# Optimization experiments

Measured on AMD Instinct MI355X. Metric: run time of the kernel, lower is better.

## Reference

```python
import jax, jax.numpy as jnp
import numpy as np

N, V = 256, 5
D_DX, D_RX = 48, 48
C = 128            # code_dim
DEMO_F, DEMO_D = 32, 64
DT, NH, DFF = 256, 8, 2048
REP, HID = 128, 256
NE, NC = 2, 64
VOC_DX = (1000, 5000, 20000)
VOC_RX = (100, 500, 2000, 5000)
NEG = -1e20

def _ln(x, s, b):
    m = jnp.mean(x, -1, keepdims=True)
    v = jnp.var(x, -1, keepdims=True)
    return (x - m) / jnp.sqrt(v + 1e-5) * s + b

def _pe(seq, d):
    pos = jnp.arange(seq, dtype=jnp.float32)[:, None]
    i = jnp.arange(0, d, 2, dtype=jnp.float32)
    ang = pos / jnp.power(10000.0, i / d)
    pe = jnp.zeros((seq, d), jnp.float32)
    pe = pe.at[:, 0::2].set(jnp.sin(ang))
    pe = pe.at[:, 1::2].set(jnp.cos(ang))
    return pe

def _mha(x, qw, qb, ow_, ob_):
    n, s, d = x.shape
    hd = d // NH
    q, k, v = jnp.split(x @ qw + qb, 3, axis=-1)
    q = q.reshape(n, s, NH, hd); k = k.reshape(n, s, NH, hd); v = v.reshape(n, s, NH, hd)
    att = jax.nn.softmax(jnp.einsum('bqhd,bkhd->bhqk', q, k) / jnp.sqrt(jnp.float32(hd)), axis=-1)
    return jnp.einsum('bhqk,bkhd->bqhd', att, v).reshape(n, s, d) @ ow_ + ob_

def _enc_layer(x, qw, qb, ow_, ob_, l1s, l1b, f1w, f1b, f2w, f2b, l2s, l2b):
    x = _ln(x + _mha(x, qw, qb, ow_, ob_), l1s, l1b)            # post-norm, as nn.TransformerEncoderLayer default
    ff = jnp.maximum(x @ f1w + f1b, 0.0) @ f2w + f2b
    return _ln(x + ff, l2s, l2b)

def setup_inputs() -> dict:
    key = jax.random.key(0)
    ks = iter(jax.random.split(key, 96))
    def nrm(shape, scale=0.02):
        return jax.random.normal(next(ks), shape, jnp.float32) * scale
    def zeros(shape): return jnp.zeros(shape, jnp.float32)
    def ones(shape): return jnp.ones(shape, jnp.float32)
    inp = {}
    inp['x_dx_l1'] = jax.random.randint(next(ks), (N, V, D_DX), 0, VOC_DX[0])
    inp['x_dx_l2'] = jax.random.randint(next(ks), (N, V, D_DX), 0, VOC_DX[1])
    inp['x_dx_l3'] = jax.random.randint(next(ks), (N, V, D_DX), 0, VOC_DX[2])
    inp['x_rx_l1'] = jax.random.randint(next(ks), (N, V, D_RX), 0, VOC_RX[0])
    inp['x_rx_l2'] = jax.random.randint(next(ks), (N, V, D_RX), 0, VOC_RX[1])
    inp['x_rx_l3'] = jax.random.randint(next(ks), (N, V, D_RX), 0, VOC_RX[2])
    inp['x_rx_l4'] = jax.random.randint(next(ks), (N, V, D_RX), 0, VOC_RX[3])
    inp['x_demo'] = jax.random.normal(next(ks), (N, V, DEMO_F), jnp.float32)
    inp['W_demo'] = nrm((DEMO_F, DEMO_D)); inp['b_demo'] = zeros((DEMO_D,))
    inp['E_dx1'] = nrm((VOC_DX[0], C)); inp['E_dx2'] = nrm((VOC_DX[1], C)); inp['E_dx3'] = nrm((VOC_DX[2], C))
    inp['E_rx1'] = nrm((VOC_RX[0], C)); inp['E_rx2'] = nrm((VOC_RX[1], C))
    inp['E_rx3'] = nrm((VOC_RX[2], C)); inp['E_rx4'] = nrm((VOC_RX[3], C))
    inp['We_dx'] = nrm((2 * C, 1)); inp['be_dx'] = zeros((1,))
    inp['We_rx'] = nrm((2 * C, 1)); inp['be_rx'] = zeros((1,))
    inp['Wev_dx'] = nrm((C, 1)); inp['bev_dx'] = zeros((1,))
    inp['Wev_rx'] = nrm((C, 1)); inp['bev_rx'] = zeros((1,))
    inp['Wcv'] = nrm((REP, 1)); inp['bcv'] = zeros((1,))
    inp['enc_w1'] = nrm((DEMO_D + C, DT)); inp['enc_b1'] = zeros((DT,))
    inp['qkv_w'] = nrm((4, DT, 3 * DT)); inp['qkv_b'] = zeros((4, 3 * DT))
    inp['ow'] = nrm((4, DT, DT)); inp['ob'] = zeros((4, DT))
    inp['ln1s'] = ones((4, DT)); inp['ln1b'] = zeros((4, DT))
    inp['ff1w'] = nrm((4, DT, DFF)); inp['ff1b'] = zeros((4, DFF))
    inp['ff2w'] = nrm((4, DFF, DT)); inp['ff2b'] = zeros((4, DT))
    inp['ln2s'] = ones((4, DT)); inp['ln2b'] = zeros((4, DT))
    inp['enc_w2'] = nrm((DT, REP)); inp['enc_b2'] = zeros((REP,))
    inp['mlp_w'] = nrm((REP, REP // 2)); inp['mlp_b'] = zeros((REP // 2,))
    inp['mlp2_w'] = nrm((REP // 2, REP // 2)); inp['mlp2_b'] = zeros((REP // 2,))
    inp['fc1w'] = nrm((NE, REP, HID)); inp['fc1b'] = zeros((NE, HID))
    inp['fc2w'] = nrm((NE, HID, HID // 2)); inp['fc2b'] = zeros((NE, HID // 2))
    inp['fc3w'] = nrm((NE, HID // 2, NC)); inp['fc3b'] = zeros((NE, NC))
    return inp

def reference(x_dx_l1, x_dx_l2, x_dx_l3, x_rx_l1, x_rx_l2, x_rx_l3, x_rx_l4, x_demo,
              W_demo, b_demo, E_dx1, E_dx2, E_dx3, E_rx1, E_rx2, E_rx3, E_rx4,
              We_dx, be_dx, We_rx, be_rx, Wev_dx, bev_dx, Wev_rx, bev_rx, Wcv, bcv,
              enc_w1, enc_b1, qkv_w, qkv_b, ow, ob, ln1s, ln1b, ff1w, ff1b, ff2w, ff2b,
              ln2s, ln2b, enc_w2, enc_b2, mlp_w, mlp_b, mlp2_w, mlp2_b,
              fc1w, fc1b, fc2w, fc2b, fc3w, fc3b):
    # ---- GRAM context vectors (dropout is identity at inference) ----
    emb_dx = jnp.stack([E_dx1[x_dx_l1], E_dx2[x_dx_l2], E_dx3[x_dx_l3]], axis=-2)          # [N,V,D,3,C]
    cat_dx = jnp.concatenate([jnp.broadcast_to(emb_dx[..., 2:3, :], emb_dx.shape), emb_dx], axis=-1)
    en_dx = jnp.maximum(cat_dx @ We_dx + be_dx, 0.0)                                       # [N,V,D,3,1]
    en_dx = jnp.where((x_dx_l1 != 0)[..., None, None], en_dx, NEG)
    att_dx = jax.nn.softmax(en_dx, axis=-2)
    cv_dx = jnp.einsum('nvdr,nvdrc->nvdc', att_dx[..., 0], emb_dx)                          # [N,V,D,C]

    emb_rx = jnp.stack([E_rx1[x_rx_l1], E_rx2[x_rx_l2], E_rx3[x_rx_l3], E_rx4[x_rx_l4]], axis=-2)  # [N,V,D,4,C]
    cat_rx = jnp.concatenate([jnp.broadcast_to(emb_rx[..., 3:4, :], emb_rx.shape), emb_rx], axis=-1)
    en_rx = jnp.maximum(cat_rx @ We_rx + be_rx, 0.0)
    en_rx = jnp.where((x_rx_l1 != 0)[..., None, None], en_rx, NEG)
    att_rx = jax.nn.softmax(en_rx, axis=-2)
    cv_rx = jnp.einsum('nvdr,nvdrc->nvdc', att_rx[..., 0], emb_rx)

    # ---- visit-level attention pooling over concatenated codes ----
    context = jnp.concatenate([cv_dx, cv_rx], axis=-2)                                      # [N,V,Ddx+Drx,C]
    ev_dx = jnp.where((x_dx_l1 != 0)[..., None], cv_dx @ Wev_dx + bev_dx, NEG)
    ev_rx = jnp.where((x_rx_l1 != 0)[..., None], cv_rx @ Wev_rx + bev_rx, NEG)
    att_v = jax.nn.softmax(jnp.concatenate([ev_dx, ev_rx], axis=-2), axis=-2)               # [N,V,M,1]
    ccv = jnp.einsum('nvm,nvmc->nvc', att_v[..., 0], context)                               # [N,V,C]

    # ---- shared transformer encoder ----
    demo = jnp.maximum(x_demo @ W_demo + b_demo, 0.0)
    x = jnp.concatenate([demo, ccv], axis=-1) @ enc_w1 + enc_b1
    x = x + _pe(V, DT)[None]
    for i in range(4):
        x = _enc_layer(x, qkv_w[i], qkv_b[i], ow[i], ob[i], ln1s[i], ln1b[i],
                       ff1w[i], ff1b[i], ff2w[i], ff2b[i], ln2s[i], ln2b[i])
    enc = x @ enc_w2 + enc_b2                                                               # [N,V,REP]

    # ---- visit compression ----
    a = jax.nn.softmax(enc @ Wcv + bcv, axis=-2)                                            # [N,V,1]
    civ = jnp.einsum('nv,nvc->nc', a[..., 0], enc)                                          # [N,REP]

    ph = jnp.maximum(civ @ mlp_w + mlp_b, 0.0) @ mlp2_w + mlp2_b                            # [N,REP/2]

    # ---- per-event FC heads (vectorized over events) ----
    h = jnp.maximum(jnp.einsum('nc,ech->neh', civ, fc1w) + fc1b, 0.0)
    h = jnp.maximum(jnp.einsum('neh,ehk->nek', h, fc2w) + fc2b, 0.0)
    out = jax.nn.sigmoid(jnp.einsum('nek,ekm->nem', h, fc3w) + fc3b)                        # [N,NE,NC]
    return out, civ, ph
```

## Files before the change

### kernel.cpp

```cpp
#include <hip/hip_runtime.h>
#include <hip/hip_bf16.h>
#include <math.h>

#define N_PAT 256
#define VIS   5
#define NV    (N_PAT*VIS)
#define DD    48
#define CD    128
#define DT    256
#define NHD   8
#define HD    32
#define DFF   2048
#define REP   128

#define GF_BIAS 1
#define GF_RELU 2
#define GF_PE   4

typedef __attribute__((ext_vector_type(8))) short short8v;
typedef __attribute__((ext_vector_type(4))) float f32x4;

__device__ __forceinline__ unsigned short f2b(float f) {
    unsigned u = __float_as_uint(f);
    return (unsigned short)((u + 0x7fffu + ((u >> 16) & 1u)) >> 16);
}

__global__ void pe_kernel(float* __restrict__ pe) {
    int pos = blockIdx.x, c = threadIdx.x;
    int j = c >> 1;
    float ang = (float)pos / powf(10000.f, (2.f * (float)j) / 256.f);
    pe[pos * DT + c] = (c & 1) ? cosf(ang) : sinf(ang);
}

__global__ __launch_bounds__(256) void wconv_kernel(
    const float* __restrict__ in, unsigned short* __restrict__ out, int K, int N)
{
    __shared__ float t[32][33];
    const float* src = in + (size_t)blockIdx.z * K * N;
    unsigned short* dst = out + (size_t)blockIdx.z * N * K;
    int k0 = blockIdx.y * 32, n0 = blockIdx.x * 32;
    int tx = threadIdx.x & 31, ty = threadIdx.x >> 5;
    #pragma unroll
    for (int r = ty; r < 32; r += 8) t[r][tx] = src[(size_t)(k0 + r) * N + n0 + tx];
    __syncthreads();
    #pragma unroll
    for (int r = ty; r < 32; r += 8) dst[(size_t)(n0 + r) * K + k0 + tx] = f2b(t[tx][r]);
}

__global__ __launch_bounds__(256) void proj_kernel(
    const float* __restrict__ E, const float* __restrict__ W_lo,
    const float* __restrict__ W_hi, const float* __restrict__ Wev,
    int nrows, float* __restrict__ out)
{
    const int row = blockIdx.x * 4 + (threadIdx.x >> 6);
    const int lane = threadIdx.x & 63;
    if (row >= nrows) return;
    float2 e   = *(const float2*)(E + (size_t)row * CD + lane * 2);
    float2 whi = *(const float2*)(W_hi + lane * 2);
    float2 wlo = *(const float2*)(W_lo + lane * 2);
    float2 wev = *(const float2*)(Wev + lane * 2);
    float ph = e.x * whi.x + e.y * whi.y;
    float pl = e.x * wlo.x + e.y * wlo.y;
    float pw = e.x * wev.x + e.y * wev.y;
    #pragma unroll
    for (int off = 32; off; off >>= 1) {
        ph += __shfl_xor(ph, off, 64);
        pl += __shfl_xor(pl, off, 64);
        pw += __shfl_xor(pw, off, 64);
    }
    if (lane == 0) {
        out[(size_t)row * 4 + 0] = ph;
        out[(size_t)row * 4 + 1] = pl;
        out[(size_t)row * 4 + 2] = pw;
        out[(size_t)row * 4 + 3] = 0.f;
    }
}

__global__ __launch_bounds__(256) void gram_kernel(
    const int* __restrict__ xd1, const int* __restrict__ xd2, const int* __restrict__ xd3,
    const int* __restrict__ xr1, const int* __restrict__ xr2, const int* __restrict__ xr3,
    const int* __restrict__ xr4,
    const float* __restrict__ Ed1, const float* __restrict__ Ed2, const float* __restrict__ Ed3,
    const float* __restrict__ Er1, const float* __restrict__ Er2, const float* __restrict__ Er3,
    const float* __restrict__ Er4,
    const float* __restrict__ pd1, const float* __restrict__ pd2, const float* __restrict__ pd3,
    const float* __restrict__ pr1, const float* __restrict__ pr2, const float* __restrict__ pr3,
    const float* __restrict__ pr4,
    const float* __restrict__ be_dx, const float* __restrict__ be_rx,
    const float* __restrict__ bev_dx, const float* __restrict__ bev_rx,
    float* __restrict__ ccv)
{
    __shared__ float aw[96][4];
    __shared__ float ev[96];
    __shared__ int   sidx[96][4];
    __shared__ float part[4][128];
    const int nv   = blockIdx.x;
    const int tid  = threadIdx.x;
    const int wave = tid >> 6, lane = tid & 63;
    const int base = nv * DD;

    if (tid < 48) {
        const int d = tid;
        const int i1 = xd1[base + d], i2 = xd2[base + d], i3 = xd3[base + d];
        sidx[d][0] = i1; sidx[d][1] = i2; sidx[d][2] = i3;
        float4 q1 = *(const float4*)(pd1 + (size_t)i1 * 4);
        float4 q2 = *(const float4*)(pd2 + (size_t)i2 * 4);
        float4 q3 = *(const float4*)(pd3 + (size_t)i3 * 4);
        const float be = be_dx[0];
        const float p0 = q3.y;
        float s1 = fmaxf(p0 + q1.x + be, 0.f);
        float s2 = fmaxf(p0 + q2.x + be, 0.f);
        float s3 = fmaxf(p0 + q3.x + be, 0.f);
        float a1, a2, a3;
        if (i1 != 0) {
            float mx = fmaxf(s1, fmaxf(s2, s3));
            a1 = expf(s1 - mx); a2 = expf(s2 - mx); a3 = expf(s3 - mx);
        } else {
            a1 = a2 = a3 = 1.f;
        }
        float inv = 1.f / (a1 + a2 + a3);
        a1 *= inv; a2 *= inv; a3 *= inv;
        aw[d][0] = a1; aw[d][1] = a2; aw[d][2] = a3; aw[d][3] = 0.f;
        ev[d] = (i1 != 0) ? (a1 * q1.z + a2 * q2.z + a3 * q3.z + bev_dx[0]) : -1e20f;
    } else if (tid >= 64 && tid < 112) {
        const int d = tid - 64;
        const int i1 = xr1[base + d], i2 = xr2[base + d], i3 = xr3[base + d], i4 = xr4[base + d];
        const int m = 48 + d;
        sidx[m][0] = i1; sidx[m][1] = i2; sidx[m][2] = i3; sidx[m][3] = i4;
        float4 q1 = *(const float4*)(pr1 + (size_t)i1 * 4);
        float4 q2 = *(const float4*)(pr2 + (size_t)i2 * 4);
        float4 q3 = *(const float4*)(pr3 + (size_t)i3 * 4);
        float4 q4 = *(const float4*)(pr4 + (size_t)i4 * 4);
        const float be = be_rx[0];
        const float p0 = q4.y;
        float s1 = fmaxf(p0 + q1.x + be, 0.f);
        float s2 = fmaxf(p0 + q2.x + be, 0.f);
        float s3 = fmaxf(p0 + q3.x + be, 0.f);
        float s4 = fmaxf(p0 + q4.x + be, 0.f);
        float a1, a2, a3, a4;
        if (i1 != 0) {
            float mx = fmaxf(fmaxf(s1, s2), fmaxf(s3, s4));
            a1 = expf(s1 - mx); a2 = expf(s2 - mx); a3 = expf(s3 - mx); a4 = expf(s4 - mx);
        } else {
            a1 = a2 = a3 = a4 = 1.f;
        }
        float inv = 1.f / (a1 + a2 + a3 + a4);
        aw[m][0] = a1 * inv; aw[m][1] = a2 * inv; aw[m][2] = a3 * inv; aw[m][3] = a4 * inv;
        ev[m] = (i1 != 0) ? ((a1 * q1.z + a2 * q2.z + a3 * q3.z + a4 * q4.z) * inv + bev_rx[0])
                          : -1e20f;
    }
    __syncthreads();

    if (wave == 0) {
        float a = ev[lane];
        float b = (lane < 32) ? ev[64 + lane] : -3.0e38f;
        float mx = fmaxf(a, b);
        #pragma unroll
        for (int off = 32; off; off >>= 1) mx = fmaxf(mx, __shfl_xor(mx, off, 64));
        float ea = expf(a - mx);
        float eb = (lane < 32) ? expf(b - mx) : 0.f;
        float s = ea + eb;
        #pragma unroll
        for (int off = 32; off; off >>= 1) s += __shfl_xor(s, off, 64);
        float inv = 1.f / s;
        ev[lane] = ea * inv;
        if (lane < 32) ev[64 + lane] = eb * inv;
    }
    __syncthreads();

    if (tid < 96) {
        float av = ev[tid];
        aw[tid][0] *= av; aw[tid][1] *= av; aw[tid][2] *= av; aw[tid][3] *= av;
    }
    __syncthreads();

    float accx = 0.f, accy = 0.f;
    const int co = lane * 2;
    for (int m = wave; m < 96; m += 4) {
        if (m < 48) {
            int i1 = sidx[m][0], i2 = sidx[m][1], i3 = sidx[m][2];
            float2 e1 = *(const float2*)(Ed1 + (size_t)i1 * CD + co);
            float2 e2 = *(const float2*)(Ed2 + (size_t)i2 * CD + co);
            float2 e3 = *(const float2*)(Ed3 + (size_t)i3 * CD + co);
            float w1 = aw[m][0], w2 = aw[m][1], w3 = aw[m][2];
            accx += w1 * e1.x + w2 * e2.x + w3 * e3.x;
            accy += w1 * e1.y + w2 * e2.y + w3 * e3.y;
        } else {
            int i1 = sidx[m][0], i2 = sidx[m][1], i3 = sidx[m][2], i4 = sidx[m][3];
            float2 e1 = *(const float2*)(Er1 + (size_t)i1 * CD + co);
            float2 e2 = *(const float2*)(Er2 + (size_t)i2 * CD + co);
            float2 e3 = *(const float2*)(Er3 + (size_t)i3 * CD + co);
            float2 e4 = *(const float2*)(Er4 + (size_t)i4 * CD + co);
            float w1 = aw[m][0], w2 = aw[m][1], w3 = aw[m][2], w4 = aw[m][3];
            accx += w1 * e1.x + w2 * e2.x + w3 * e3.x + w4 * e4.x;
            accy += w1 * e1.y + w2 * e2.y + w3 * e3.y + w4 * e4.y;
        }
    }
    part[wave][co]     = accx;
    part[wave][co + 1] = accy;
    __syncthreads();
    if (tid < CD) {
        ccv[(size_t)nv * CD + tid] =
            part[0][tid] + part[1][tid] + part[2][tid] + part[3][tid];
    }
}

__global__ __launch_bounds__(192) void build_x0(
    const float* __restrict__ x_demo, const float* __restrict__ W_demo,
    const float* __restrict__ b_demo, const float* __restrict__ ccv,
    unsigned short* __restrict__ A0bf)
{
    int row = blockIdx.x, j = threadIdx.x;
    float v;
    if (j < 64) {
        float acc = b_demo[j];
        #pragma unroll
        for (int f = 0; f < 32; ++f) acc += x_demo[row * 32 + f] * W_demo[f * 64 + j];
        v = fmaxf(acc, 0.f);
    } else {
        v = ccv[row * CD + (j - 64)];
    }
    A0bf[row * 192 + j] = f2b(v);
}

__global__ __launch_bounds__(256) void gemm_bf(
    const unsigned short* __restrict__ A, const unsigned short* __restrict__ B,
    const float* __restrict__ bias, const float* __restrict__ pe,
    float* __restrict__ Cf, unsigned short* __restrict__ Cb,
    int M, int N, int K, int flags, int kchunk)
{
    __shared__ unsigned short As[64][40];
    __shared__ unsigned short Bs[64][40];
    const int bm = blockIdx.y * 64, bn = blockIdx.x * 64;
    const int tid = threadIdx.x;
    const int wave = tid >> 6, lane = tid & 63;
    const int wr = (wave >> 1) * 32, wc = (wave & 1) * 32;
    const int l15 = lane & 15, l4 = lane >> 4;
    const int srow = tid >> 2, sk8 = (tid & 3) * 8;
    const int kbeg = blockIdx.z * kchunk, kend = kbeg + kchunk;
    f32x4 acc[2][2] = {};

    for (int k0 = kbeg; k0 < kend; k0 += 32) {
        *(short8v*)&As[srow][sk8] = *(const short8v*)(A + (size_t)(bm + srow) * K + k0 + sk8);
        *(short8v*)&Bs[srow][sk8] = *(const short8v*)(B + (size_t)(bn + srow) * K + k0 + sk8);
        __syncthreads();
        short8v a0 = *(const short8v*)&As[wr + l15][l4 * 8];
        short8v a1 = *(const short8v*)&As[wr + 16 + l15][l4 * 8];
        short8v b0 = *(const short8v*)&Bs[wc + l15][l4 * 8];
        short8v b1 = *(const short8v*)&Bs[wc + 16 + l15][l4 * 8];
        acc[0][0] = __builtin_amdgcn_mfma_f32_16x16x32_bf16(a0, b0, acc[0][0], 0, 0, 0);
        acc[0][1] = __builtin_amdgcn_mfma_f32_16x16x32_bf16(a0, b1, acc[0][1], 0, 0, 0);
        acc[1][0] = __builtin_amdgcn_mfma_f32_16x16x32_bf16(a1, b0, acc[1][0], 0, 0, 0);
        acc[1][1] = __builtin_amdgcn_mfma_f32_16x16x32_bf16(a1, b1, acc[1][1], 0, 0, 0);
        __syncthreads();
    }

    if (gridDim.z == 1) {
        #pragma unroll
        for (int mi = 0; mi < 2; ++mi)
            #pragma unroll
            for (int ni = 0; ni < 2; ++ni) {
                int col = bn + wc + ni * 16 + l15;
                float bz = (flags & GF_BIAS) ? bias[col] : 0.f;
                #pragma unroll
                for (int r = 0; r < 4; ++r) {
                    int row = bm + wr + mi * 16 + l4 * 4 + r;
                    float v = acc[mi][ni][r] + bz;
                    if (flags & GF_PE)   v += pe[(row % VIS) * N + col];
                    if (flags & GF_RELU) v = fmaxf(v, 0.f);
                    if (Cf) Cf[(size_t)row * N + col] = v;
                    if (Cb) Cb[(size_t)row * N + col] = f2b(v);
                }
            }
    } else {
        float* Cp = Cf + (size_t)blockIdx.z * M * N;
        #pragma unroll
        for (int mi = 0; mi < 2; ++mi)
            #pragma unroll
            for (int ni = 0; ni < 2; ++ni) {
                int col = bn + wc + ni * 16 + l15;
                #pragma unroll
                for (int r = 0; r < 4; ++r) {
                    int row = bm + wr + mi * 16 + l4 * 4 + r;
                    Cp[(size_t)row * N + col] = acc[mi][ni][r];
                }
            }
    }
}

__global__ __launch_bounds__(256) void gemm_k(
    const float* __restrict__ A, const float* __restrict__ B,
    const float* __restrict__ bias, const float* __restrict__ pe,
    float* __restrict__ C, int M, int N, int K, int flags, int kchunk)
{
    __shared__ float As[16][68];
    __shared__ float Bs[16][64];
    const int bm = blockIdx.y * 64, bn = blockIdx.x * 64;
    const int tid = threadIdx.x;
    const int tx = tid & 15, ty = tid >> 4;
    const int kbeg = blockIdx.z * kchunk;
    const int kend = kbeg + kchunk;
    const int ar  = tid >> 2, akc = (tid & 3) * 4;
    const int bbr = tid >> 4, bbc = (tid & 15) * 4;
    float acc[4][4] = {{0.f}};

    for (int k0 = kbeg; k0 < kend; k0 += 16) {
        float4 va = *(const float4*)(A + (size_t)(bm + ar) * K + k0 + akc);
        float4 vb = *(const float4*)(B + (size_t)(k0 + bbr) * N + bn + bbc);
        As[akc + 0][ar] = va.x;
        As[akc + 1][ar] = va.y;
        As[akc + 2][ar] = va.z;
        As[akc + 3][ar] = va.w;
        *(float4*)&Bs[bbr][bbc] = vb;
        __syncthreads();
        #pragma unroll
        for (int kk = 0; kk < 16; ++kk) {
            float4 a = *(const float4*)&As[kk][ty * 4];
            float4 b = *(const float4*)&Bs[kk][tx * 4];
            acc[0][0] += a.x * b.x; acc[0][1] += a.x * b.y; acc[0][2] += a.x * b.z; acc[0][3] += a.x * b.w;
            acc[1][0] += a.y * b.x; acc[1][1] += a.y * b.y; acc[1][2] += a.y * b.z; acc[1][3] += a.y * b.w;
            acc[2][0] += a.z * b.x; acc[2][1] += a.z * b.y; acc[2][2] += a.z * b.z; acc[2][3] += a.z * b.w;
            acc[3][0] += a.w * b.x; acc[3][1] += a.w * b.y; acc[3][2] += a.w * b.z; acc[3][3] += a.w * b.w;
        }
        __syncthreads();
    }

    if (gridDim.z == 1) {
        #pragma unroll
        for (int i = 0; i < 4; ++i) {
            int row = bm + ty * 4 + i;
            int col0 = bn + tx * 4;
            float4 v = *(float4*)&acc[i][0];
            if (flags & GF_BIAS) {
                const float4 bz = *(const float4*)(bias + col0);
                v.x += bz.x; v.y += bz.y; v.z += bz.z; v.w += bz.w;
            }
            if (flags & GF_PE) {
                const float4 pz = *(const float4*)(pe + (row % VIS) * N + col0);
                v.x += pz.x; v.y += pz.y; v.z += pz.z; v.w += pz.w;
            }
            if (flags & GF_RELU) {
                v.x = fmaxf(v.x, 0.f); v.y = fmaxf(v.y, 0.f);
                v.z = fmaxf(v.z, 0.f); v.w = fmaxf(v.w, 0.f);
            }
            *(float4*)(C + (size_t)row * N + col0) = v;
        }
    } else {
        float* Cp = C + (size_t)blockIdx.z * M * N;
        #pragma unroll
        for (int i = 0; i < 4; ++i) {
            int row = bm + ty * 4 + i;
            *(float4*)(Cp + (size_t)row * N + bn + tx * 4) = *(float4*)&acc[i][0];
        }
    }
}

__global__ void reduce_kernel(
    const float* __restrict__ part, int S, int MN,
    const float* __restrict__ bias,
    const float* __restrict__ resid,
    const float* __restrict__ lns, const float* __restrict__ lnb,
    int N, float* __restrict__ out, unsigned short* __restrict__ out_bf)
{
    const int row = blockIdx.x, t = threadIdx.x;
    const size_t idx = (size_t)row * N + t;
    float v = bias[t];
    for (int s = 0; s < S; ++s) v += part[(size_t)s * MN + idx];
    if (resid) v += resid[idx];
    if (lns) {
        float s1 = v, s2 = v * v;
        #pragma unroll
        for (int off = 32; off; off >>= 1) {
            s1 += __shfl_xor(s1, off, 64);
            s2 += __shfl_xor(s2, off, 64);
        }
        __shared__ float red[2][4];
        const int wave = t >> 6, lane = t & 63, nw = blockDim.x >> 6;
        if (lane == 0) { red[0][wave] = s1; red[1][wave] = s2; }
        __syncthreads();
        s1 = 0.f; s2 = 0.f;
        for (int w = 0; w < nw; ++w) { s1 += red[0][w]; s2 += red[1][w]; }
        float invn = 1.f / (float)N;
        float m    = s1 * invn;
        float var  = s2 * invn - m * m;
        float inv  = 1.f / sqrtf(var + 1e-5f);
        v = (v - m) * inv * lns[t] + lnb[t];
    }
    out[idx] = v;
    if (out_bf) out_bf[idx] = f2b(v);
}

__global__ __launch_bounds__(256) void attn_kernel(
    const float* __restrict__ qkv, unsigned short* __restrict__ out)
{
    const int n = blockIdx.x;
    const int tid = threadIdx.x;
    const int h = tid >> 5, t = tid & 31;
    const int ch = h * HD + t;
    float q[VIS], k[VIS], v[VIS];
    #pragma unroll
    for (int j = 0; j < VIS; ++j) {
        const float* row = qkv + (size_t)(n * VIS + j) * 768 + ch;
        q[j] = row[0]; k[j] = row[256]; v[j] = row[512];
    }
    const float scale = 0.1767766952966369f;
    float sm[VIS][VIS];
    #pragma unroll
    for (int qi = 0; qi < VIS; ++qi)
        #pragma unroll
        for (int ki = 0; ki < VIS; ++ki) {
            float p = q[qi] * k[ki];
            #pragma unroll
            for (int off = 16; off; off >>= 1) p += __shfl_xor(p, off, 32);
            sm[qi][ki] = p * scale;
        }
    #pragma unroll
    for (int qi = 0; qi < VIS; ++qi) {
        float mx = sm[qi][0];
        #pragma unroll
        for (int ki = 1; ki < VIS; ++ki) mx = fmaxf(mx, sm[qi][ki]);
        float e[VIS], sum = 0.f;
        #pragma unroll
        for (int ki = 0; ki < VIS; ++ki) { e[ki] = expf(sm[qi][ki] - mx); sum += e[ki]; }
        float inv = 1.f / sum;
        float acc = 0.f;
        #pragma unroll
        for (int ki = 0; ki < VIS; ++ki) acc += e[ki] * inv * v[ki];
        out[(size_t)(n * VIS + qi) * DT + ch] = f2b(acc);
    }
}

__global__ __launch_bounds__(128) void vc_ph_kernel(
    const float* __restrict__ enc, const float* __restrict__ Wcv, const float* __restrict__ bcv,
    const float* __restrict__ mlp_w, const float* __restrict__ mlp_b,
    const float* __restrict__ mlp2_w, const float* __restrict__ mlp2_b,
    float* __restrict__ civ_out, float* __restrict__ ph_out)
{
    const int n = blockIdx.x, t = threadIdx.x;
    const int wave = t >> 6, lane = t & 63;
    float e[VIS];
    #pragma unroll
    for (int v = 0; v < VIS; ++v) e[v] = enc[(size_t)(n * VIS + v) * REP + t];
    float w = Wcv[t];
    __shared__ float part[VIS][2];
    #pragma unroll
    for (int v = 0; v < VIS; ++v) {
        float pv = e[v] * w;
        #pragma unroll
        for (int off = 32; off; off >>= 1) pv += __shfl_xor(pv, off, 64);
        if (lane == 0) part[v][wave] = pv;
    }
    __syncthreads();
    float b0 = bcv[0];
    float sc[VIS], mx = -3e38f;
    #pragma unroll
    for (int v = 0; v < VIS; ++v) { sc[v] = part[v][0] + part[v][1] + b0; mx = fmaxf(mx, sc[v]); }
    float sum = 0.f;
    #pragma unroll
    for (int v = 0; v < VIS; ++v) { sc[v] = expf(sc[v] - mx); sum += sc[v]; }
    float inv = 1.f / sum;
    float civ = 0.f;
    #pragma unroll
    for (int v = 0; v < VIS; ++v) civ += sc[v] * inv * e[v];
    civ_out[(size_t)n * REP + t] = civ;

    __shared__ float civ_s[REP];
    __shared__ float h1_s[64];
    civ_s[t] = civ;
    __syncthreads();
    if (t < 64) {
        float acc = mlp_b[t];
        #pragma unroll 8
        for (int c = 0; c < REP; ++c) acc += civ_s[c] * mlp_w[c * 64 + t];
        h1_s[t] = fmaxf(acc, 0.f);
    }
    __syncthreads();
    if (t < 64) {
        float acc = mlp2_b[t];
        #pragma unroll 8
        for (int j = 0; j < 64; ++j) acc += h1_s[j] * mlp2_w[j * 64 + t];
        ph_out[(size_t)n * 64 + t] = acc;
    }
}

__global__ __launch_bounds__(256) void heads_kernel(
    const float* __restrict__ civ,
    const float* __restrict__ fc1w, const float* __restrict__ fc1b,
    const float* __restrict__ fc2w, const float* __restrict__ fc2b,
    const float* __restrict__ fc3w, const float* __restrict__ fc3b,
    float* __restrict__ out)
{
    const int n = blockIdx.x >> 1, e = blockIdx.x & 1;
    const int t = threadIdx.x;
    __shared__ float civ_s[REP], h1[256], h2[128];
    if (t < REP) civ_s[t] = civ[(size_t)n * REP + t];
    __syncthreads();
    {
        float acc = fc1b[e * 256 + t];
        const float* w = fc1w + (size_t)e * REP * 256;
        #pragma unroll 8
        for (int c = 0; c < REP; ++c) acc += civ_s[c] * w[c * 256 + t];
        h1[t] = fmaxf(acc, 0.f);
    }
    __syncthreads();
    if (t < 128) {
        float acc = fc2b[e * 128 + t];
        const float* w = fc2w + (size_t)e * 256 * 128;
        #pragma unroll 8
        for (int c = 0; c < 256; ++c) acc += h1[c] * w[c * 128 + t];
        h2[t] = fmaxf(acc, 0.f);
    }
    __syncthreads();
    if (t < 64) {
        float acc = fc3b[e * 64 + t];
        const float* w = fc3w + (size_t)e * 128 * 64;
        #pragma unroll 8
        for (int c = 0; c < 128; ++c) acc += h2[c] * w[c * 64 + t];
        out[(size_t)(n * 2 + e) * 64 + t] = 1.f / (1.f + expf(-acc));
    }
}

extern "C" void kernel_launch(void* const* d_in, const int* in_sizes, int n_in,
                              void* d_out, int out_size, void* d_ws, size_t ws_size,
                              hipStream_t stream) {
    const int*   xd1    = (const int*)  d_in[0];
    const int*   xd2    = (const int*)  d_in[1];
    const int*   xd3    = (const int*)  d_in[2];
    const int*   xr1    = (const int*)  d_in[3];
    const int*   xr2    = (const int*)  d_in[4];
    const int*   xr3    = (const int*)  d_in[5];
    const int*   xr4    = (const int*)  d_in[6];
    const float* x_demo = (const float*)d_in[7];
    const float* W_demo = (const float*)d_in[8];
    const float* b_demo = (const float*)d_in[9];
    const float* Ed1    = (const float*)d_in[10];
    const float* Ed2    = (const float*)d_in[11];
    const float* Ed3    = (const float*)d_in[12];
    const float* Er1    = (const float*)d_in[13];
    const float* Er2    = (const float*)d_in[14];
    const float* Er3    = (const float*)d_in[15];
    const float* Er4    = (const float*)d_in[16];
    const float* We_dx  = (const float*)d_in[17];
    const float* be_dx  = (const float*)d_in[18];
    const float* We_rx  = (const float*)d_in[19];
    const float* be_rx  = (const float*)d_in[20];
    const float* Wev_dx = (const float*)d_in[21];
    const float* bev_dx = (const float*)d_in[22];
    const float* Wev_rx = (const float*)d_in[23];
    const float* bev_rx = (const float*)d_in[24];
    const float* Wcv    = (const float*)d_in[25];
    const float* bcv    = (const float*)d_in[26];
    const float* enc_w1 = (const float*)d_in[27];
    const float* enc_b1 = (const float*)d_in[28];
    const float* qkv_w  = (const float*)d_in[29];
    const float* qkv_b  = (const float*)d_in[30];
    const float* ow     = (const float*)d_in[31];
    const float* ob     = (const float*)d_in[32];
    const float* ln1s   = (const float*)d_in[33];
    const float* ln1b   = (const float*)d_in[34];
    const float* ff1w   = (const float*)d_in[35];
    const float* ff1b   = (const float*)d_in[36];
    const float* ff2w   = (const float*)d_in[37];
    const float* ff2b   = (const float*)d_in[38];
    const float* ln2s   = (const float*)d_in[39];
    const float* ln2b   = (const float*)d_in[40];
    const float* enc_w2 = (const float*)d_in[41];
    const float* enc_b2 = (const float*)d_in[42];
    const float* mlp_w  = (const float*)d_in[43];
    const float* mlp_b  = (const float*)d_in[44];
    const float* mlp2_w = (const float*)d_in[45];
    const float* mlp2_b = (const float*)d_in[46];
    const float* fc1w   = (const float*)d_in[47];
    const float* fc1b   = (const float*)d_in[48];
    const float* fc2w   = (const float*)d_in[49];
    const float* fc2b   = (const float*)d_in[50];
    const float* fc3w   = (const float*)d_in[51];
    const float* fc3b   = (const float*)d_in[52];

    float* ws     = (float*)d_ws;
    float* pe     = ws;
    float* ccv    = pe + 1280;
    float* xbuf   = ccv + 163840;
    float* qkvbuf = xbuf + 327680;
    float* projbf = qkvbuf + 983040;
    float* enc    = projbf + 327680;
    float* buf2   = enc + 163840;
    float* ptab   = buf2 + 1310720;
    unsigned short* usb = (unsigned short*)(ptab + 134400);
    unsigned short* A0bf    = usb;
    unsigned short* xbuf_bf = A0bf + 245760;
    unsigned short* attn_bf = xbuf_bf + 327680;
    unsigned short* ff1_bf  = attn_bf + 327680;
    unsigned short* qkv_wt  = ff1_bf + 2621440;
    unsigned short* ow_t    = qkv_wt + 786432;
    unsigned short* ff1_wt  = ow_t + 262144;
    unsigned short* ff2_wt  = ff1_wt + 2097152;
    unsigned short* ew1_t   = ff2_wt + 2097152;

    float* pd1 = ptab;
    float* pd2 = pd1 + 4000;
    float* pd3 = pd2 + 20000;
    float* pr1 = pd3 + 80000;
    float* pr2 = pr1 + 400;
    float* pr3 = pr2 + 2000;
    float* pr4 = pr3 + 8000;

    pe_kernel<<<VIS, DT, 0, stream>>>(pe);

    wconv_kernel<<<dim3(24, 8, 4), 256, 0, stream>>>(qkv_w, qkv_wt, 256, 768);
    wconv_kernel<<<dim3(8, 8, 4), 256, 0, stream>>>(ow, ow_t, 256, 256);
    wconv_kernel<<<dim3(64, 8, 4), 256, 0, stream>>>(ff1w, ff1_wt, 256, 2048);
    wconv_kernel<<<dim3(8, 64, 4), 256, 0, stream>>>(ff2w, ff2_wt, 2048, 256);
    wconv_kernel<<<dim3(8, 6, 1), 256, 0, stream>>>(enc_w1, ew1_t, 192, 256);

    proj_kernel<<<(1000 + 3) / 4, 256, 0, stream>>>(Ed1, We_dx, We_dx + CD, Wev_dx, 1000, pd1);
    proj_kernel<<<(5000 + 3) / 4, 256, 0, stream>>>(Ed2, We_dx, We_dx + CD, Wev_dx, 5000, pd2);
    proj_kernel<<<(20000 + 3) / 4, 256, 0, stream>>>(Ed3, We_dx, We_dx + CD, Wev_dx, 20000, pd3);
    proj_kernel<<<(100 + 3) / 4, 256, 0, stream>>>(Er1, We_rx, We_rx + CD, Wev_rx, 100, pr1);
    proj_kernel<<<(500 + 3) / 4, 256, 0, stream>>>(Er2, We_rx, We_rx + CD, Wev_rx, 500, pr2);
    proj_kernel<<<(2000 + 3) / 4, 256, 0, stream>>>(Er3, We_rx, We_rx + CD, Wev_rx, 2000, pr3);
    proj_kernel<<<(5000 + 3) / 4, 256, 0, stream>>>(Er4, We_rx, We_rx + CD, Wev_rx, 5000, pr4);

    gram_kernel<<<NV, 256, 0, stream>>>(xd1, xd2, xd3, xr1, xr2, xr3, xr4,
                                        Ed1, Ed2, Ed3, Er1, Er2, Er3, Er4,
                                        pd1, pd2, pd3, pr1, pr2, pr3, pr4,
                                        be_dx, be_rx, bev_dx, bev_rx, ccv);
    build_x0<<<NV, 192, 0, stream>>>(x_demo, W_demo, b_demo, ccv, A0bf);

    gemm_bf<<<dim3(4, 20, 1), 256, 0, stream>>>(A0bf, ew1_t, enc_b1, pe,
                                                xbuf, xbuf_bf, NV, DT, 192,
                                                GF_BIAS | GF_PE, 192);

    for (int i = 0; i < 4; ++i) {
        gemm_bf<<<dim3(12, 20, 1), 256, 0, stream>>>(
            xbuf_bf, qkv_wt + (size_t)i * 768 * 256, qkv_b + i * 768, nullptr,
            qkvbuf, nullptr, NV, 768, DT, GF_BIAS, DT);
        attn_kernel<<<N_PAT, 256, 0, stream>>>(qkvbuf, attn_bf);
        gemm_bf<<<dim3(4, 20, 1), 256, 0, stream>>>(
            attn_bf, ow_t + (size_t)i * 256 * 256, nullptr, nullptr,
            projbf, nullptr, NV, DT, DT, 0, DT);
        reduce_kernel<<<NV, DT, 0, stream>>>(projbf, 1, NV * DT, ob + i * DT,
                                             xbuf, ln1s + i * DT, ln1b + i * DT,
                                             DT, xbuf, xbuf_bf);
        gemm_bf<<<dim3(32, 20, 1), 256, 0, stream>>>(
            xbuf_bf, ff1_wt + (size_t)i * DFF * 256, ff1b + i * DFF, nullptr,
            nullptr, ff1_bf, NV, DFF, DT, GF_BIAS | GF_RELU, DT);
        gemm_bf<<<dim3(4, 20, 4), 256, 0, stream>>>(
            ff1_bf, ff2_wt + (size_t)i * 256 * DFF, nullptr, nullptr,
            buf2, nullptr, NV, DT, DFF, 0, 512);
        reduce_kernel<<<NV, DT, 0, stream>>>(buf2, 4, NV * DT, ff2b + i * DT,
                                             xbuf, ln2s + i * DT, ln2b + i * DT,
                                             DT, xbuf, xbuf_bf);
    }

    gemm_k<<<dim3(2, 20, 8), 256, 0, stream>>>(xbuf, enc_w2, nullptr, nullptr, buf2,
                                               NV, REP, DT, 0, 32);
    reduce_kernel<<<NV, REP, 0, stream>>>(buf2, 8, NV * REP, enc_b2,
                                          nullptr, nullptr, nullptr, REP, enc, nullptr);

    float* civ_out = (float*)d_out + 32768;
    float* ph_out  = (float*)d_out + 65536;
    vc_ph_kernel<<<N_PAT, 128, 0, stream>>>(enc, Wcv, bcv, mlp_w, mlp_b, mlp2_w, mlp2_b,
                                            civ_out, ph_out);
    heads_kernel<<<N_PAT * 2, 256, 0, stream>>>(civ_out, fc1w, fc1b, fc2w, fc2b, fc3w, fc3b,
                                                (float*)d_out);
}
```

Measured before the change: 477.8 us.

## Fuse prep kernels, attention with out-proj and LayerNorm, and final reduce

Merges the PE and seven projection launches into one prep kernel, and the weight conversions into one batched launch that drops the out-proj conversion. Build_x0 is folded into gram_kernel. The attention kernel now also does the out-projection in fp32 from shared memory plus bias, residual and LayerNorm, replacing an MFMA GEMM and a reduce launch per layer. The final split-K reduce moves into vc_ph_kernel. This cuts launch count and intermediate buffers, but the out-projection now runs as scalar FP32 FMAs on one block per patient (256 blocks) instead of matrix cores.

```diff
diff --git a/kernel.cpp b/kernel.cpp
--- a/kernel.cpp
+++ b/kernel.cpp
@@ -8,7 +8,6 @@
 #define DD    48
 #define CD    128
 #define DT    256
-#define NHD   8
 #define HD    32
 #define DFF   2048
 #define REP   128
@@ -25,39 +24,41 @@
     return (unsigned short)((u + 0x7fffu + ((u >> 16) & 1u)) >> 16);
 }
 
-__global__ void pe_kernel(float* __restrict__ pe) {
-    int pos = blockIdx.x, c = threadIdx.x;
-    int j = c >> 1;
-    float ang = (float)pos / powf(10000.f, (2.f * (float)j) / 256.f);
-    pe[pos * DT + c] = (c & 1) ? cosf(ang) : sinf(ang);
-}
-
-__global__ __launch_bounds__(256) void wconv_kernel(
-    const float* __restrict__ in, unsigned short* __restrict__ out, int K, int N)
-{
-    __shared__ float t[32][33];
-    const float* src = in + (size_t)blockIdx.z * K * N;
-    unsigned short* dst = out + (size_t)blockIdx.z * N * K;
-    int k0 = blockIdx.y * 32, n0 = blockIdx.x * 32;
-    int tx = threadIdx.x & 31, ty = threadIdx.x >> 5;
-    #pragma unroll
-    for (int r = ty; r < 32; r += 8) t[r][tx] = src[(size_t)(k0 + r) * N + n0 + tx];
-    __syncthreads();
-    #pragma unroll
-    for (int r = ty; r < 32; r += 8) dst[(size_t)(n0 + r) * K + k0 + tx] = f2b(t[tx][r]);
-}
-
-__global__ __launch_bounds__(256) void proj_kernel(
-    const float* __restrict__ E, const float* __restrict__ W_lo,
-    const float* __restrict__ W_hi, const float* __restrict__ Wev,
-    int nrows, float* __restrict__ out)
-{
-    const int row = blockIdx.x * 4 + (threadIdx.x >> 6);
+__global__ __launch_bounds__(256) void prep_kernel(
+    const float* __restrict__ Ed1, const float* __restrict__ Ed2, const float* __restrict__ Ed3,
+    const float* __restrict__ Er1, const float* __restrict__ Er2, const float* __restrict__ Er3,
+    const float* __restrict__ Er4,
+    const float* __restrict__ We_dx, const float* __restrict__ We_rx,
+    const float* __restrict__ Wev_dx, const float* __restrict__ Wev_rx,
+    float* __restrict__ pe,
+    float* __restrict__ pd1, float* __restrict__ pd2, float* __restrict__ pd3,
+    float* __restrict__ pr1, float* __restrict__ pr2, float* __restrict__ pr3,
+    float* __restrict__ pr4)
+{
+    const int b = blockIdx.x;
+    if (b < VIS) {
+        int c = threadIdx.x, j = c >> 1;
+        float ang = (float)b / powf(10000.f, (2.f * (float)j) / 256.f);
+        pe[b * DT + c] = (c & 1) ? cosf(ang) : sinf(ang);
+        return;
+    }
+    const int g = (b - VIS) * 4 + (threadIdx.x >> 6);
     const int lane = threadIdx.x & 63;
-    if (row >= nrows) return;
-    float2 e   = *(const float2*)(E + (size_t)row * CD + lane * 2);
-    float2 whi = *(const float2*)(W_hi + lane * 2);
-    float2 wlo = *(const float2*)(W_lo + lane * 2);
+    if (g >= 33600) return;
+    const float* E; float* out; int loc; int isdx;
+    if      (g < 1000)  { E = Ed1; out = pd1; loc = g;          isdx = 1; }
+    else if (g < 6000)  { E = Ed2; out = pd2; loc = g - 1000;   isdx = 1; }
+    else if (g < 26000) { E = Ed3; out = pd3; loc = g - 6000;   isdx = 1; }
+    else if (g < 26100) { E = Er1; out = pr1; loc = g - 26000;  isdx = 0; }
+    else if (g < 26600) { E = Er2; out = pr2; loc = g - 26100;  isdx = 0; }
+    else if (g < 28600) { E = Er3; out = pr3; loc = g - 26600;  isdx = 0; }
+    else                { E = Er4; out = pr4; loc = g - 28600;  isdx = 0; }
+    const float* Wlo = isdx ? We_dx : We_rx;
+    const float* Whi = Wlo + CD;
+    const float* Wev = isdx ? Wev_dx : Wev_rx;
+    float2 e   = *(const float2*)(E + (size_t)loc * CD + lane * 2);
+    float2 whi = *(const float2*)(Whi + lane * 2);
+    float2 wlo = *(const float2*)(Wlo + lane * 2);
     float2 wev = *(const float2*)(Wev + lane * 2);
     float ph = e.x * whi.x + e.y * whi.y;
     float pl = e.x * wlo.x + e.y * wlo.y;
@@ -69,11 +70,46 @@
         pw += __shfl_xor(pw, off, 64);
     }
     if (lane == 0) {
-        out[(size_t)row * 4 + 0] = ph;
-        out[(size_t)row * 4 + 1] = pl;
-        out[(size_t)row * 4 + 2] = pw;
-        out[(size_t)row * 4 + 3] = 0.f;
-    }
+        out[(size_t)loc * 4 + 0] = ph;
+        out[(size_t)loc * 4 + 1] = pl;
+        out[(size_t)loc * 4 + 2] = pw;
+        out[(size_t)loc * 4 + 3] = 0.f;
+    }
+}
+
+__global__ __launch_bounds__(256) void wconv_all(
+    const float* __restrict__ qkv_w, unsigned short* __restrict__ qkv_wt,
+    const float* __restrict__ ff1w,  unsigned short* __restrict__ ff1_wt,
+    const float* __restrict__ ff2w,  unsigned short* __restrict__ ff2_wt,
+    const float* __restrict__ ew1,   unsigned short* __restrict__ ew1_t)
+{
+    __shared__ float t[32][33];
+    int b = blockIdx.x;
+    const float* src; unsigned short* dst; int K, N, ky, nx;
+    if (b < 768) {
+        int mat = b / 192, r = b % 192; ky = r / 24; nx = r % 24;
+        K = 256; N = 768;
+        src = qkv_w + (size_t)mat * K * N; dst = qkv_wt + (size_t)mat * N * K;
+    } else if (b < 2816) {
+        b -= 768; int mat = b / 512, r = b % 512; ky = r / 64; nx = r % 64;
+        K = 256; N = 2048;
+        src = ff1w + (size_t)mat * K * N; dst = ff1_wt + (size_t)mat * N * K;
+    } else if (b < 4864) {
+        b -= 2816; int mat = b / 512, r = b % 512; ky = r / 8; nx = r % 8;
+        K = 2048; N = 256;
+        src = ff2w + (size_t)mat * K * N; dst = ff2_wt + (size_t)mat * N * K;
+    } else {
+        b -= 4864; ky = b / 8; nx = b % 8;
+        K = 192; N = 256;
+        src = ew1; dst = ew1_t;
+    }
+    int k0 = ky * 32, n0 = nx * 32;
+    int tx = threadIdx.x & 31, ty = threadIdx.x >> 5;
+    #pragma unroll
+    for (int r = ty; r < 32; r += 8) t[r][tx] = src[(size_t)(k0 + r) * N + n0 + tx];
+    __syncthreads();
+    #pragma unroll
+    for (int r = ty; r < 32; r += 8) dst[(size_t)(n0 + r) * K + k0 + tx] = f2b(t[tx][r]);
 }
 
 __global__ __launch_bounds__(256) void gram_kernel(
@@ -88,7 +124,9 @@
     const float* __restrict__ pr4,
     const float* __restrict__ be_dx, const float* __restrict__ be_rx,
     const float* __restrict__ bev_dx, const float* __restrict__ bev_rx,
-    float* __restrict__ ccv)
+    const float* __restrict__ x_demo, const float* __restrict__ W_demo,
+    const float* __restrict__ b_demo,
+    unsigned short* __restrict__ A0bf)
 {
     __shared__ float aw[96][4];
     __shared__ float ev[96];
@@ -200,27 +238,15 @@
     part[wave][co + 1] = accy;
     __syncthreads();
     if (tid < CD) {
-        ccv[(size_t)nv * CD + tid] =
-            part[0][tid] + part[1][tid] + part[2][tid] + part[3][tid];
-    }
-}
-
-__global__ __launch_bounds__(192) void build_x0(
-    const float* __restrict__ x_demo, const float* __restrict__ W_demo,
-    const float* __restrict__ b_demo, const float* __restrict__ ccv,
-    unsigned short* __restrict__ A0bf)
-{
-    int row = blockIdx.x, j = threadIdx.x;
-    float v;
-    if (j < 64) {
+        A0bf[(size_t)nv * 192 + 64 + tid] =
+            f2b(part[0][tid] + part[1][tid] + part[2][tid] + part[3][tid]);
+    } else if (tid >= 192) {
+        int j = tid - 192;
         float acc = b_demo[j];
         #pragma unroll
-        for (int f = 0; f < 32; ++f) acc += x_demo[row * 32 + f] * W_demo[f * 64 + j];
-        v = fmaxf(acc, 0.f);
-    } else {
-        v = ccv[row * CD + (j - 64)];
-    }
-    A0bf[row * 192 + j] = f2b(v);
+        for (int f = 0; f < 32; ++f) acc += x_demo[nv * 32 + f] * W_demo[f * 64 + j];
+        A0bf[(size_t)nv * 192 + j] = f2b(fmaxf(acc, 0.f));
+    }
 }
 
 __global__ __launch_bounds__(256) void gemm_bf(
@@ -290,8 +316,7 @@
 
 __global__ __launch_bounds__(256) void gemm_k(
     const float* __restrict__ A, const float* __restrict__ B,
-    const float* __restrict__ bias, const float* __restrict__ pe,
-    float* __restrict__ C, int M, int N, int K, int flags, int kchunk)
+    float* __restrict__ C, int M, int N, int K, int kchunk)
 {
     __shared__ float As[16][68];
     __shared__ float Bs[16][64];
@@ -325,33 +350,11 @@
         __syncthreads();
     }
 
-    if (gridDim.z == 1) {
-        #pragma unroll
-        for (int i = 0; i < 4; ++i) {
-            int row = bm + ty * 4 + i;
-            int col0 = bn + tx * 4;
-            float4 v = *(float4*)&acc[i][0];
-            if (flags & GF_BIAS) {
-                const float4 bz = *(const float4*)(bias + col0);
-                v.x += bz.x; v.y += bz.y; v.z += bz.z; v.w += bz.w;
-            }
-            if (flags & GF_PE) {
-                const float4 pz = *(const float4*)(pe + (row % VIS) * N + col0);
-                v.x += pz.x; v.y += pz.y; v.z += pz.z; v.w += pz.w;
-            }
-            if (flags & GF_RELU) {
-                v.x = fmaxf(v.x, 0.f); v.y = fmaxf(v.y, 0.f);
-                v.z = fmaxf(v.z, 0.f); v.w = fmaxf(v.w, 0.f);
-            }
-            *(float4*)(C + (size_t)row * N + col0) = v;
-        }
-    } else {
-        float* Cp = C + (size_t)blockIdx.z * M * N;
-        #pragma unroll
-        for (int i = 0; i < 4; ++i) {
-            int row = bm + ty * 4 + i;
-            *(float4*)(Cp + (size_t)row * N + bn + tx * 4) = *(float4*)&acc[i][0];
-        }
+    float* Cp = C + (size_t)blockIdx.z * M * N;
+    #pragma unroll
+    for (int i = 0; i < 4; ++i) {
+        int row = bm + ty * 4 + i;
+        *(float4*)(Cp + (size_t)row * N + bn + tx * 4) = *(float4*)&acc[i][0];
     }
 }
 
@@ -390,48 +393,98 @@
     if (out_bf) out_bf[idx] = f2b(v);
 }
 
-__global__ __launch_bounds__(256) void attn_kernel(
-    const float* __restrict__ qkv, unsigned short* __restrict__ out)
-{
+__global__ __launch_bounds__(256) void attn_proj_ln(
+    const float* __restrict__ qkv,
+    const float* __restrict__ ow,
+    const float* __restrict__ ob,
+    const float* __restrict__ lns, const float* __restrict__ lnb,
+    float* __restrict__ xbuf, unsigned short* __restrict__ xbuf_bf)
+{
+    __shared__ float attn_s[VIS][DT];
+    __shared__ float red[VIS][2][4];
     const int n = blockIdx.x;
     const int tid = threadIdx.x;
     const int h = tid >> 5, t = tid & 31;
     const int ch = h * HD + t;
-    float q[VIS], k[VIS], v[VIS];
+
+    {
+        float q[VIS], k[VIS], v[VIS];
+        #pragma unroll
+        for (int j = 0; j < VIS; ++j) {
+            const float* row = qkv + (size_t)(n * VIS + j) * 768 + ch;
+            q[j] = row[0]; k[j] = row[256]; v[j] = row[512];
+        }
+        const float scale = 0.1767766952966369f;
+        float sm[VIS][VIS];
+        #pragma unroll
+        for (int qi = 0; qi < VIS; ++qi)
+            #pragma unroll
+            for (int ki = 0; ki < VIS; ++ki) {
+                float p = q[qi] * k[ki];
+                #pragma unroll
+                for (int off = 16; off; off >>= 1) p += __shfl_xor(p, off, 32);
+                sm[qi][ki] = p * scale;
+            }
+        #pragma unroll
+        for (int qi = 0; qi < VIS; ++qi) {
+            float mx = sm[qi][0];
+            #pragma unroll
+            for (int ki = 1; ki < VIS; ++ki) mx = fmaxf(mx, sm[qi][ki]);
+            float e[VIS], sum = 0.f;
+            #pragma unroll
+            for (int ki = 0; ki < VIS; ++ki) { e[ki] = expf(sm[qi][ki] - mx); sum += e[ki]; }
+            float inv = 1.f / sum;
+            float acc = 0.f;
+            #pragma unroll
+            for (int ki = 0; ki < VIS; ++ki) acc += e[ki] * inv * v[ki];
+            attn_s[qi][ch] = acc;
+        }
+    }
+    __syncthreads();
+
+    const int c = tid;
+    float acc[VIS] = {0.f, 0.f, 0.f, 0.f, 0.f};
+    #pragma unroll 4
+    for (int k = 0; k < DT; ++k) {
+        float w = ow[(size_t)k * DT + c];
+        #pragma unroll
+        for (int j = 0; j < VIS; ++j) acc[j] += attn_s[j][k] * w;
+    }
+    float bz = ob[c];
+    float v[VIS];
+    #pragma unroll
+    for (int j = 0; j < VIS; ++j)
+        v[j] = acc[j] + bz + xbuf[(size_t)(n * VIS + j) * DT + c];
+
+    const int wave = tid >> 6, lane = tid & 63;
     #pragma unroll
     for (int j = 0; j < VIS; ++j) {
-        const float* row = qkv + (size_t)(n * VIS + j) * 768 + ch;
-        q[j] = row[0]; k[j] = row[256]; v[j] = row[512];
-    }
-    const float scale = 0.1767766952966369f;
-    float sm[VIS][VIS];
-    #pragma unroll
-    for (int qi = 0; qi < VIS; ++qi)
-        #pragma unroll
-        for (int ki = 0; ki < VIS; ++ki) {
-            float p = q[qi] * k[ki];
-            #pragma unroll
-            for (int off = 16; off; off >>= 1) p += __shfl_xor(p, off, 32);
-            sm[qi][ki] = p * scale;
+        float s1 = v[j], s2 = v[j] * v[j];
+        #pragma unroll
+        for (int off = 32; off; off >>= 1) {
+            s1 += __shfl_xor(s1, off, 64);
+            s2 += __shfl_xor(s2, off, 64);
         }
-    #pragma unroll
-    for (int qi = 0; qi < VIS; ++qi) {
-        float mx = sm[qi][0];
-        #pragma unroll
-        for (int ki = 1; ki < VIS; ++ki) mx = fmaxf(mx, sm[qi][ki]);
-        float e[VIS], sum = 0.f;
-        #pragma unroll
-        for (int ki = 0; ki < VIS; ++ki) { e[ki] = expf(sm[qi][ki] - mx); sum += e[ki]; }
-        float inv = 1.f / sum;
-        float acc = 0.f;
-        #pragma unroll
-        for (int ki = 0; ki < VIS; ++ki) acc += e[ki] * inv * v[ki];
-        out[(size_t)(n * VIS + qi) * DT + ch] = f2b(acc);
+        if (lane == 0) { red[j][0][wave] = s1; red[j][1][wave] = s2; }
+    }
+    __syncthreads();
+    #pragma unroll
+    for (int j = 0; j < VIS; ++j) {
+        float s1 = red[j][0][0] + red[j][0][1] + red[j][0][2] + red[j][0][3];
+        float s2 = red[j][1][0] + red[j][1][1] + red[j][1][2] + red[j][1][3];
+        float m   = s1 * (1.f / 256.f);
+        float var = s2 * (1.f / 256.f) - m * m;
+        float inv = 1.f / sqrtf(var + 1e-5f);
+        float o = (v[j] - m) * inv * lns[c] + lnb[c];
+        size_t idx = (size_t)(n * VIS + j) * DT + c;
+        xbuf[idx] = o;
+        xbuf_bf[idx] = f2b(o);
     }
 }
 
 __global__ __launch_bounds__(128) void vc_ph_kernel(
-    const float* __restrict__ enc, const float* __restrict__ Wcv, const float* __restrict__ bcv,
+    const float* __restrict__ encp, int S, int MN, const float* __restrict__ enc_b2,
+    const float* __restrict__ Wcv, const float* __restrict__ bcv,
     const float* __restrict__ mlp_w, const float* __restrict__ mlp_b,
     const float* __restrict__ mlp2_w, const float* __restrict__ mlp2_b,
     float* __restrict__ civ_out, float* __restrict__ ph_out)
@@ -440,7 +493,12 @@
     const int wave = t >> 6, lane = t & 63;
     float e[VIS];
     #pragma unroll
-    for (int v = 0; v < VIS; ++v) e[v] = enc[(size_t)(n * VIS + v) * REP + t];
+    for (int v = 0; v < VIS; ++v) {
+        size_t idx = (size_t)(n * VIS + v) * REP + t;
+        float ev = enc_b2[t];
+        for (int s = 0; s < S; ++s) ev += encp[(size_t)s * MN + idx];
+        e[v] = ev;
+    }
     float w = Wcv[t];
     __shared__ float part[VIS][2];
     #pragma unroll
@@ -579,21 +637,16 @@
 
     float* ws     = (float*)d_ws;
     float* pe     = ws;
-    float* ccv    = pe + 1280;
-    float* xbuf   = ccv + 163840;
+    float* xbuf   = pe + 1280;
     float* qkvbuf = xbuf + 327680;
-    float* projbf = qkvbuf + 983040;
-    float* enc    = projbf + 327680;
-    float* buf2   = enc + 163840;
+    float* buf2   = qkvbuf + 983040;
     float* ptab   = buf2 + 1310720;
     unsigned short* usb = (unsigned short*)(ptab + 134400);
     unsigned short* A0bf    = usb;
     unsigned short* xbuf_bf = A0bf + 245760;
-    unsigned short* attn_bf = xbuf_bf + 327680;
-    unsigned short* ff1_bf  = attn_bf + 327680;
+    unsigned short* ff1_bf  = xbuf_bf + 327680;
     unsigned short* qkv_wt  = ff1_bf + 2621440;
-    unsigned short* ow_t    = qkv_wt + 786432;
-    unsigned short* ff1_wt  = ow_t + 262144;
+    unsigned short* ff1_wt  = qkv_wt + 786432;
     unsigned short* ff2_wt  = ff1_wt + 2097152;
     unsigned short* ew1_t   = ff2_wt + 2097152;
 
@@ -605,27 +658,16 @@
     float* pr3 = pr2 + 2000;
     float* pr4 = pr3 + 8000;
 
-    pe_kernel<<<VIS, DT, 0, stream>>>(pe);
-
-    wconv_kernel<<<dim3(24, 8, 4), 256, 0, stream>>>(qkv_w, qkv_wt, 256, 768);
-    wconv_kernel<<<dim3(8, 8, 4), 256, 0, stream>>>(ow, ow_t, 256, 256);
-    wconv_kernel<<<dim3(64, 8, 4), 256, 0, stream>>>(ff1w, ff1_wt, 256, 2048);
-    wconv_kernel<<<dim3(8, 64, 4), 256, 0, stream>>>(ff2w, ff2_wt, 2048, 256);
-    wconv_kernel<<<dim3(8, 6, 1), 256, 0, stream>>>(enc_w1, ew1_t, 192, 256);
-
-    proj_kernel<<<(1000 + 3) / 4, 256, 0, stream>>>(Ed1, We_dx, We_dx + CD, Wev_dx, 1000, pd1);
-    proj_kernel<<<(5000 + 3) / 4, 256, 0, stream>>>(Ed2, We_dx, We_dx + CD, Wev_dx, 5000, pd2);
-    proj_kernel<<<(20000 + 3) / 4, 256, 0, stream>>>(Ed3, We_dx, We_dx + CD, Wev_dx, 20000, pd3);
-    proj_kernel<<<(100 + 3) / 4, 256, 0, stream>>>(Er1, We_rx, We_rx + CD, Wev_rx, 100, pr1);
-    proj_kernel<<<(500 + 3) / 4, 256, 0, stream>>>(Er2, We_rx, We_rx + CD, Wev_rx, 500, pr2);
-    proj_kernel<<<(2000 + 3) / 4, 256, 0, stream>>>(Er3, We_rx, We_rx + CD, Wev_rx, 2000, pr3);
-    proj_kernel<<<(5000 + 3) / 4, 256, 0, stream>>>(Er4, We_rx, We_rx + CD, Wev_rx, 5000, pr4);
-
+    prep_kernel<<<5 + 8400, 256, 0, stream>>>(Ed1, Ed2, Ed3, Er1, Er2, Er3, Er4,
+                                              We_dx, We_rx, Wev_dx, Wev_rx,
+                                              pe, pd1, pd2, pd3, pr1, pr2, pr3, pr4);
+    wconv_all<<<4912, 256, 0, stream>>>(qkv_w, qkv_wt, ff1w, ff1_wt, ff2w, ff2_wt,
+                                        enc_w1, ew1_t);
     gram_kernel<<<NV, 256, 0, stream>>>(xd1, xd2, xd3, xr1, xr2, xr3, xr4,
                                         Ed1, Ed2, Ed3, Er1, Er2, Er3, Er4,
                                         pd1, pd2, pd3, pr1, pr2, pr3, pr4,
-                                        be_dx, be_rx, bev_dx, bev_rx, ccv);
-    build_x0<<<NV, 192, 0, stream>>>(x_demo, W_demo, b_demo, ccv, A0bf);
+                                        be_dx, be_rx, bev_dx, bev_rx,
+                                        x_demo, W_demo, b_demo, A0bf);
 
     gemm_bf<<<dim3(4, 20, 1), 256, 0, stream>>>(A0bf, ew1_t, enc_b1, pe,
                                                 xbuf, xbuf_bf, NV, DT, 192,
@@ -635,13 +677,9 @@
         gemm_bf<<<dim3(12, 20, 1), 256, 0, stream>>>(
             xbuf_bf, qkv_wt + (size_t)i * 768 * 256, qkv_b + i * 768, nullptr,
             qkvbuf, nullptr, NV, 768, DT, GF_BIAS, DT);
-        attn_kernel<<<N_PAT, 256, 0, stream>>>(qkvbuf, attn_bf);
-        gemm_bf<<<dim3(4, 20, 1), 256, 0, stream>>>(
-            attn_bf, ow_t + (size_t)i * 256 * 256, nullptr, nullptr,
-            projbf, nullptr, NV, DT, DT, 0, DT);
-        reduce_kernel<<<NV, DT, 0, stream>>>(projbf, 1, NV * DT, ob + i * DT,
-                                             xbuf, ln1s + i * DT, ln1b + i * DT,
-                                             DT, xbuf, xbuf_bf);
+        attn_proj_ln<<<N_PAT, 256, 0, stream>>>(
+            qkvbuf, ow + (size_t)i * DT * DT, ob + i * DT,
+            ln1s + i * DT, ln1b + i * DT, xbuf, xbuf_bf);
         gemm_bf<<<dim3(32, 20, 1), 256, 0, stream>>>(
             xbuf_bf, ff1_wt + (size_t)i * DFF * 256, ff1b + i * DFF, nullptr,
             nullptr, ff1_bf, NV, DFF, DT, GF_BIAS | GF_RELU, DT);
@@ -653,14 +691,12 @@
                                              DT, xbuf, xbuf_bf);
     }
 
-    gemm_k<<<dim3(2, 20, 8), 256, 0, stream>>>(xbuf, enc_w2, nullptr, nullptr, buf2,
-                                               NV, REP, DT, 0, 32);
-    reduce_kernel<<<NV, REP, 0, stream>>>(buf2, 8, NV * REP, enc_b2,
-                                          nullptr, nullptr, nullptr, REP, enc, nullptr);
+    gemm_k<<<dim3(2, 20, 8), 256, 0, stream>>>(xbuf, enc_w2, buf2, NV, REP, DT, 32);
 
     float* civ_out = (float*)d_out + 32768;
     float* ph_out  = (float*)d_out + 65536;
-    vc_ph_kernel<<<N_PAT, 128, 0, stream>>>(enc, Wcv, bcv, mlp_w, mlp_b, mlp2_w, mlp2_b,
+    vc_ph_kernel<<<N_PAT, 128, 0, stream>>>(buf2, 8, NV * REP, enc_b2,
+                                            Wcv, bcv, mlp_w, mlp_b, mlp2_w, mlp2_b,
                                             civ_out, ph_out);
     heads_kernel<<<N_PAT * 2, 256, 0, stream>>>(civ_out, fc1w, fc1b, fc2w, fc2b, fc3w, fc3b,
                                                 (float*)d_out);
```

Result: no change. 480.4 us (median of 2 runs) (+0.5%).
